# Kernel tuning notes

Measured on AMD Instinct MI355X. Metric: run time of the kernel, lower is better.

Reference implementation:

```python
import jax, jax.numpy as jnp
import numpy as np

DA, DZ, HID, IM = 5, 10, 128, 64


def _encode(x, w1, b1, w2, b2, w3, b3, wd, bd):
    # Conv2D k=4 s=2 'same' (pad 1,1) + ReLU, x3, then flatten + Dense(20)
    dn = ('NHWC', 'HWIO', 'NHWC')
    for w, b in ((w1, b1), (w2, b2), (w3, b3)):
        x = jax.lax.conv_general_dilated(x, w, (2, 2), [(1, 1), (1, 1)], dimension_numbers=dn)
        x = jax.nn.relu(x + b)
    x = x.reshape(x.shape[0], -1)
    return x @ wd + bd


def _lstm(a_in, k, rk, b):
    # keras LSTM, gate order i,f,c,o; stateful step-by-step == scan over shifted seq
    B = a_in.shape[0]
    def step(carry, x):
        h, c = carry
        g = x @ k + h @ rk + b
        gi, gf, gg, go = jnp.split(g, 4, axis=-1)
        c = jax.nn.sigmoid(gf) * c + jax.nn.sigmoid(gi) * jnp.tanh(gg)
        h = jax.nn.sigmoid(go) * jnp.tanh(c)
        return (h, c), h
    z = jnp.zeros((B, HID), a_in.dtype)
    _, hs = jax.lax.scan(step, (z, z), jnp.swapaxes(a_in, 0, 1))
    return hs  # [T, B, HID]


def _forward(images, w1, b1, w2, b2, w3, b3, wd, bd, lk, lrk, lb, wabc, babc):
    B, T = images.shape[0], images.shape[1]
    # encode all frames in one batched pass (per-frame encode is recursion-independent)
    lat = _encode(images.reshape(B * T, IM, IM, 1), w1, b1, w2, b2, w3, b3, wd, bd)
    a_all = lat[:, :DA].reshape(B, T, DA)  # encode() mean split
    # LSTM consumes a_prev: a0=zeros at t=0, then a_{t-1}
    a_in = jnp.concatenate([jnp.zeros((B, 1, DA), a_all.dtype), a_all[:, :-1]], axis=1)
    hs = _lstm(a_in, lk, lrk, lb)  # [T,B,HID]
    abc = hs @ wabc + babc  # [T,B,DZ*DZ+DA*DZ]
    A = abc[..., :DZ * DZ].reshape(T, B, DZ, DZ)
    C = abc[..., DZ * DZ:].reshape(T, B, DA, DZ)

    Q = 0.08 * jnp.eye(DZ, dtype=a_all.dtype)
    R = 0.03 * jnp.eye(DA, dtype=a_all.dtype)
    I = jnp.eye(DZ, dtype=a_all.dtype)
    std_min = 1e-4 * I

    def kf(carry, inp):
        z, P = carry
        At, Ct, at = inp
        z_hat = jnp.einsum('bij,bj->bi', At, z)
        P_hat = At @ P @ jnp.swapaxes(At, -1, -2) + Q
        resid = at - jnp.einsum('bij,bj->bi', Ct, z_hat)
        S = Ct @ P_hat @ jnp.swapaxes(Ct, -1, -2) + R
        K = P_hat @ jnp.swapaxes(Ct, -1, -2) @ jnp.linalg.inv(S)
        pz = z_hat + jnp.einsum('bij,bj->bi', K, resid)
        pP = (I - K @ Ct) @ P_hat
        # note: clamped P_hat is stored, but update() above used the unclamped one
        return (pz, pP), (z_hat, jnp.maximum(P_hat, std_min), pz, pP)

    z0 = jnp.zeros((B, DZ), a_all.dtype)
    P0 = jnp.broadcast_to(I, (B, DZ, DZ))
    _, (z_hat_s, P_hat_s, pz_s, pP_s) = jax.lax.scan(kf, (z0, P0), (A, C, jnp.swapaxes(a_all, 0, 1)))
    last_z, last_P = pz_s[-1], pP_s[-1]

    def rts(carry, inp):
        zs, Ps = carry
        pz_prev, pP_prev, Aj, zhj, Phj = inp
        D = pP_prev @ jnp.swapaxes(Aj, -1, -2) @ jnp.linalg.inv(Phj)
        zn = pz_prev + jnp.einsum('bij,bj->bi', D, zs - zhj)
        Pn = pP_prev + D @ (Ps - Phj) @ jnp.swapaxes(D, -1, -2)
        return (zn, Pn), (zn, Pn)

    # j = T-1 .. 1, reading post[j-1], A[j], z_hat[j], P_hat_clamped[j]
    rev = (pz_s[:-1][::-1], pP_s[:-1][::-1], A[1:][::-1], z_hat_s[1:][::-1], P_hat_s[1:][::-1])
    _, (zsm_r, Psm_r) = jax.lax.scan(rts, (last_z, last_P), rev)
    z_smooth = jnp.swapaxes(zsm_r[::-1], 0, 1)  # [B, T-1, DZ]
    P_smooth = jnp.swapaxes(Psm_r[::-1], 0, 1)  # [B, T-1, DZ, DZ]
    return z_smooth, P_smooth, a_all, A, C, last_z, last_P


def setup_inputs() -> dict:
    key = jax.random.key(0)
    ks = jax.random.split(key, 9)
    B, T = 3, 128
    f = lambda k, shape, s: jax.random.normal(k, shape, jnp.float32) * s
    return {
        'images': jax.random.uniform(ks[0], (B, T, IM, IM, 1), jnp.float32),
        'w1': f(ks[1], (4, 4, 1, 64), 0.25), 'b1': jnp.zeros((64,), jnp.float32),
        'w2': f(ks[2], (4, 4, 64, 128), 0.03), 'b2': jnp.zeros((128,), jnp.float32),
        'w3': f(ks[3], (4, 4, 128, 512), 0.022), 'b3': jnp.zeros((512,), jnp.float32),
        'wd': f(ks[4], (8 * 8 * 512, 20), 0.006), 'bd': jnp.zeros((20,), jnp.float32),
        'lk': f(ks[5], (DA, 4 * HID), 0.3), 'lrk': f(ks[6], (HID, 4 * HID), 0.08),
        'lb': jnp.zeros((4 * HID,), jnp.float32),
        'wabc': f(ks[7], (HID, DZ * DZ + DA * DZ), 0.02),
        'babc': jnp.zeros((DZ * DZ + DA * DZ,), jnp.float32),
    }


def reference(images, w1, b1, w2, b2, w3, b3, wd, bd, lk, lrk, lb, wabc, babc):
    return _forward(images, w1, b1, w2, b2, w3, b3, wd, bd, lk, lrk, lb, wabc, babc)
```

## Files before the change

### kernel.cpp

```cpp
#include <hip/hip_runtime.h>
#include <math.h>

typedef unsigned int   u32;
typedef unsigned short u16;
typedef short bf16x8 __attribute__((ext_vector_type(8)));
typedef float f32x4  __attribute__((ext_vector_type(4)));

#define OUT_ZS    0
#define OUT_PS    3810
#define OUT_AALL  41910
#define OUT_A     43830
#define OUT_C     82230
#define OUT_LASTZ 101430
#define OUT_LASTP 101460

__device__ __forceinline__ float sigm(float x){ return 1.f/(1.f+expf(-x)); }
__device__ __forceinline__ float safed(float d){
    return (fabsf(d) < 1e-30f) ? ((d < 0.f) ? -1e-30f : 1e-30f) : d;
}
__device__ __forceinline__ u16 f2b(float f) {
    union { float f; u32 u; } v; v.f = f;
    u32 r = v.u + 0x7fffu + ((v.u >> 16) & 1u);
    return (u16)(r >> 16);
}
__device__ __forceinline__ float b2f(u16 u) {
    union { u32 x; float f; } v; v.x = ((u32)u) << 16; return v.f;
}
__device__ __forceinline__ u32 packb(float a, float b){ return (u32)f2b(a) | ((u32)f2b(b) << 16); }

__device__ u16   r14_c1[25165824];
__device__ u16   r14_c2[12582912];
__device__ u16   r14_w2h[131072];
__device__ u16   r14_w2l[131072];
__device__ u16   r14_w3h[1048576];
__device__ u16   r14_w3l[1048576];
__device__ float r14_wdT[163840];
__device__ float r20_dpart[7680];
__device__ float r14_hs[49152];
__device__ float r14_zhat[3840];
__device__ float r14_phat[38400];
__device__ float r14_pz[3840];
__device__ float r14_pp[38400];
__device__ float r14_aall[1920];
__device__ float r14_A[38400];
__device__ float r14_C[19200];
__device__ float r14_G[38400];

__global__ __launch_bounds__(256) void conv1_r14(const float* __restrict__ img,
        const float* __restrict__ w1, const float* __restrict__ b1, u16* __restrict__ out)
{
    __shared__ float in_lds[66*66];
    const int f = blockIdx.x, tid = threadIdx.x;
    const int og = tid >> 5, sg = tid & 31;

    for (int i = tid; i < 66*66; i += 256) in_lds[i] = 0.f;
    __syncthreads();
    const float4* src = (const float4*)(img + f*4096);
    for (int i = tid; i < 1024; i += 256) {
        int r = i >> 4, c0 = (i & 15) * 4;
        float4 v = src[i];
        float* dst = &in_lds[(r+1)*66 + c0 + 1];
        dst[0]=v.x; dst[1]=v.y; dst[2]=v.z; dst[3]=v.w;
    }
    float wr[16][8];
    #pragma unroll
    for (int k = 0; k < 16; k++) {
        float4 a = *(const float4*)&w1[k*64 + og*8];
        float4 b = *(const float4*)&w1[k*64 + og*8 + 4];
        wr[k][0]=a.x; wr[k][1]=a.y; wr[k][2]=a.z; wr[k][3]=a.w;
        wr[k][4]=b.x; wr[k][5]=b.y; wr[k][6]=b.z; wr[k][7]=b.w;
    }
    float bias[8];
    #pragma unroll
    for (int j = 0; j < 8; j++) bias[j] = b1[og*8+j];
    __syncthreads();

    for (int yy = 0; yy < 32; yy++) {
        float inv[16];
        #pragma unroll
        for (int ky = 0; ky < 4; ky++)
            #pragma unroll
            for (int kx = 0; kx < 4; kx++)
                inv[ky*4+kx] = in_lds[(2*yy+ky)*66 + 2*sg+kx];
        float acc[8];
        #pragma unroll
        for (int j = 0; j < 8; j++) acc[j] = bias[j];
        #pragma unroll
        for (int k = 0; k < 16; k++)
            #pragma unroll
            for (int j = 0; j < 8; j++) acc[j] += inv[k]*wr[k][j];
        #pragma unroll
        for (int j = 0; j < 8; j++) acc[j] = fmaxf(acc[j], 0.f);
        uint4 pk = make_uint4(packb(acc[0],acc[1]), packb(acc[2],acc[3]),
                              packb(acc[4],acc[5]), packb(acc[6],acc[7]));
        *(uint4*)(out + (f*1024 + yy*32 + sg)*64 + og*8) = pk;
    }
}

__global__ __launch_bounds__(256) void w2t_r14(const float* __restrict__ w2,
        u16* __restrict__ hi, u16* __restrict__ lo)
{
    int idx = blockIdx.x*256 + threadIdx.x;
    if (idx < 131072) {
        int k = idx >> 7, oc = idx & 127;
        float v = w2[idx];
        u16 h = f2b(v);
        hi[oc*1024 + k] = h;
        lo[oc*1024 + k] = f2b(v - b2f(h));
    }
}
__global__ __launch_bounds__(256) void w3t_r14(const float* __restrict__ w3,
        u16* __restrict__ hi, u16* __restrict__ lo)
{
    int idx = blockIdx.x*256 + threadIdx.x;
    if (idx < 1048576) {
        int k = idx >> 9, oc = idx & 511;
        float v = w3[idx];
        u16 h = f2b(v);
        hi[oc*2048 + k] = h;
        lo[oc*2048 + k] = f2b(v - b2f(h));
    }
}
__global__ __launch_bounds__(256) void wdt_r14(const float* __restrict__ wd, float* __restrict__ wdT)
{
    int idx = blockIdx.x*256 + threadIdx.x;
    if (idx < 163840) {
        int j = idx & 32767, d = idx >> 15;
        wdT[d*32768 + j] = wd[j*20 + d];
    }
}

__global__ __launch_bounds__(256) void conv2_r14(const u16* __restrict__ c1b,
        const u16* __restrict__ w2h, const u16* __restrict__ w2l,
        const float* __restrict__ b2, u16* __restrict__ c2b)
{
    __shared__ __align__(16) u16 slab[128*72];
    const int f = blockIdx.x, mc = blockIdx.y, tid = threadIdx.x;
    const int wave = tid >> 6, lane = tid & 63, quad = lane >> 4, ln = lane & 15;

    f32x4 acc[8][2];
    const f32x4 zz = {0.f, 0.f, 0.f, 0.f};
    #pragma unroll
    for (int mt = 0; mt < 8; mt++) { acc[mt][0] = zz; acc[mt][1] = zz; }

    const int sp = tid >> 1;
    const int sy = mc*8 + (sp >> 4), sx = sp & 15;
    const int sic = (tid & 1) * 32;

    for (int kk = 0; kk < 16; kk++) {
        const int ky = kk >> 2, kx = kk & 3;
        __syncthreads();
        {
            int iy = 2*sy - 1 + ky, ix = 2*sx - 1 + kx;
            uint4* d4 = (uint4*)&slab[sp*72 + sic];
            if (iy >= 0 && iy < 32 && ix >= 0 && ix < 32) {
                const uint4* s4 = (const uint4*)&c1b[((f*32 + iy)*32 + ix)*64 + sic];
                d4[0]=s4[0]; d4[1]=s4[1]; d4[2]=s4[2]; d4[3]=s4[3];
            } else {
                uint4 z = make_uint4(0,0,0,0);
                d4[0]=z; d4[1]=z; d4[2]=z; d4[3]=z;
            }
        }
        __syncthreads();
        #pragma unroll
        for (int ks = 0; ks < 2; ks++) {
            bf16x8 af[8];
            #pragma unroll
            for (int mt = 0; mt < 8; mt++)
                af[mt] = *(const bf16x8*)&slab[(mt*16 + ln)*72 + ks*32 + quad*8];
            #pragma unroll
            for (int nt = 0; nt < 2; nt++) {
                const int oc = wave*32 + nt*16 + ln;
                const int kb = kk*64 + ks*32 + quad*8;
                bf16x8 bh = *(const bf16x8*)&w2h[oc*1024 + kb];
                bf16x8 bl = *(const bf16x8*)&w2l[oc*1024 + kb];
                #pragma unroll
                for (int mt = 0; mt < 8; mt++) {
                    acc[mt][nt] = __builtin_amdgcn_mfma_f32_16x16x32_bf16(af[mt], bh, acc[mt][nt], 0,0,0);
                    acc[mt][nt] = __builtin_amdgcn_mfma_f32_16x16x32_bf16(af[mt], bl, acc[mt][nt], 0,0,0);
                }
            }
        }
    }
    #pragma unroll
    for (int nt = 0; nt < 2; nt++) {
        const int oc = wave*32 + nt*16 + ln;
        const float bias = b2[oc];
        #pragma unroll
        for (int mt = 0; mt < 8; mt++)
            #pragma unroll
            for (int r = 0; r < 4; r++) {
                int pix = mc*128 + mt*16 + quad*4 + r;
                c2b[(f*256 + pix)*128 + oc] = f2b(fmaxf(acc[mt][nt][r] + bias, 0.f));
            }
    }
}

__global__ __launch_bounds__(256, 3) void conv3_r21(const u16* __restrict__ c2b,
        const u16* __restrict__ w3h, const u16* __restrict__ w3l,
        const float* __restrict__ b3)
{
    __shared__ __align__(16) u16 slab[2][64*136];
    const int fp = blockIdx.x, ocg = blockIdx.y, tid = threadIdx.x;
    const int wave = tid >> 6, lane = tid & 63, quad = lane >> 4, ln = lane & 15;
    const int wn = ocg*128 + wave*32;

    f32x4 acc[2][4][2];
    const f32x4 zz = {0.f, 0.f, 0.f, 0.f};
    #pragma unroll
    for (int f2 = 0; f2 < 2; f2++)
        #pragma unroll
        for (int mt = 0; mt < 4; mt++) { acc[f2][mt][0] = zz; acc[f2][mt][1] = zz; }

    const int sp = tid >> 2;
    const int sy = sp >> 3, sx = sp & 7;
    const int sic = (tid & 3) * 32;

    for (int kk = 0; kk < 16; kk++) {
        const int ky = kk >> 2, kx = kk & 3;
        const int iy = 2*sy - 1 + ky, ix = 2*sx - 1 + kx;
        const bool vin = (iy >= 0 && iy < 16 && ix >= 0 && ix < 16);
        __syncthreads();
        #pragma unroll
        for (int f2 = 0; f2 < 2; f2++) {
            const int f = fp*2 + f2;
            uint4* d4 = (uint4*)&slab[f2][sp*136 + sic];
            if (vin) {
                const uint4* s4 = (const uint4*)&c2b[((f*16 + iy)*16 + ix)*128 + sic];
                d4[0]=s4[0]; d4[1]=s4[1]; d4[2]=s4[2]; d4[3]=s4[3];
            } else {
                uint4 z = make_uint4(0,0,0,0);
                d4[0]=z; d4[1]=z; d4[2]=z; d4[3]=z;
            }
        }
        __syncthreads();
        #pragma unroll
        for (int ks = 0; ks < 4; ks++) {
            bf16x8 af[2][4];
            #pragma unroll
            for (int f2 = 0; f2 < 2; f2++)
                #pragma unroll
                for (int mt = 0; mt < 4; mt++)
                    af[f2][mt] = *(const bf16x8*)&slab[f2][(mt*16 + ln)*136 + ks*32 + quad*8];
            const int kb = kk*128 + ks*32 + quad*8;
            #pragma unroll
            for (int nt = 0; nt < 2; nt++) {
                const int oc = wn + nt*16 + ln;
                bf16x8 bh = *(const bf16x8*)&w3h[oc*2048 + kb];
                bf16x8 bl = *(const bf16x8*)&w3l[oc*2048 + kb];
                #pragma unroll
                for (int f2 = 0; f2 < 2; f2++)
                    #pragma unroll
                    for (int mt = 0; mt < 4; mt++) {
                        acc[f2][mt][nt] = __builtin_amdgcn_mfma_f32_16x16x32_bf16(af[f2][mt], bh, acc[f2][mt][nt], 0,0,0);
                        acc[f2][mt][nt] = __builtin_amdgcn_mfma_f32_16x16x32_bf16(af[f2][mt], bl, acc[f2][mt][nt], 0,0,0);
                    }
            }
        }
    }

    float pd[2][5];
    #pragma unroll
    for (int f2 = 0; f2 < 2; f2++)
        #pragma unroll
        for (int d = 0; d < 5; d++) pd[f2][d] = 0.f;
    #pragma unroll
    for (int nt = 0; nt < 2; nt++) {
        const int oc = wn + nt*16 + ln;
        const float bias = b3[oc];
        #pragma unroll
        for (int mt = 0; mt < 4; mt++)
            #pragma unroll
            for (int r = 0; r < 4; r++) {
                const int pix = mt*16 + quad*4 + r;
                const float* wp = &r14_wdT[pix*512 + oc];
                const float w0 = wp[0], w1 = wp[32768], w2 = wp[65536],
                            w3v = wp[98304], w4 = wp[131072];
                #pragma unroll
                for (int f2 = 0; f2 < 2; f2++) {
                    const float v = fmaxf(acc[f2][mt][nt][r] + bias, 0.f);
                    pd[f2][0] += v*w0; pd[f2][1] += v*w1; pd[f2][2] += v*w2;
                    pd[f2][3] += v*w3v; pd[f2][4] += v*w4;
                }
            }
    }
    __syncthreads();
    float* red = (float*)slab;
    #pragma unroll
    for (int f2 = 0; f2 < 2; f2++)
        #pragma unroll
        for (int d = 0; d < 5; d++) red[(f2*5+d)*256 + tid] = pd[f2][d];
    __syncthreads();
    for (int st = 128; st > 0; st >>= 1) {
        if (tid < st) {
            #pragma unroll
            for (int q = 0; q < 10; q++) red[q*256+tid] += red[q*256+tid+st];
        }
        __syncthreads();
    }
    if (tid < 10) {
        const int f2 = tid/5, d = tid%5;
        r20_dpart[((fp*2+f2)*4 + ocg)*5 + d] = red[tid*256];
    }
}

__global__ __launch_bounds__(512) void lstm_r21(const float* __restrict__ lk,
        const float* __restrict__ lrk, const float* __restrict__ lb,
        const float* __restrict__ bd, float* __restrict__ dout)
{
    const int b = blockIdx.x, c = threadIdx.x;
    __shared__ float a_lds[640];
    __shared__ float h_lds[128];
    __shared__ float g_lds[512];
    for (int i = c; i < 640; i += 512) {
        const int f = b*128 + i/5, d = i % 5;
        float v = bd[d];
        #pragma unroll
        for (int g = 0; g < 4; g++) v += r20_dpart[f*20 + g*5 + d];
        a_lds[i] = v;
        r14_aall[f*5 + d] = v;
        dout[OUT_AALL + f*5 + d] = v;
    }
    if (c < 128) h_lds[c] = 0.f;
    float wreg[128];
    #pragma unroll
    for (int j = 0; j < 128; j++) wreg[j] = lrk[j*512 + c];
    float lkr[5];
    #pragma unroll
    for (int d = 0; d < 5; d++) lkr[d] = lk[d*512 + c];
    const float gb = lb[c];
    float cs = 0.f;
    __syncthreads();
    for (int t = 0; t < 128; t++) {
        float g = gb;
        if (t > 0) {
            #pragma unroll
            for (int d = 0; d < 5; d++) g += a_lds[(t-1)*5 + d] * lkr[d];
        }
        float s0=0.f, s1=0.f, s2=0.f, s3=0.f;
        #pragma unroll
        for (int j = 0; j < 128; j += 4) {
            float4 h4 = *(const float4*)&h_lds[j];
            s0 += h4.x*wreg[j];   s1 += h4.y*wreg[j+1];
            s2 += h4.z*wreg[j+2]; s3 += h4.w*wreg[j+3];
        }
        g += (s0 + s1) + (s2 + s3);
        g_lds[c] = g;
        __syncthreads();
        if (c < 128) {
            float gi = g_lds[c], gf = g_lds[c+128], gg = g_lds[c+256], go = g_lds[c+384];
            cs = sigm(gf)*cs + sigm(gi)*tanhf(gg);
            float hn = sigm(go)*tanhf(cs);
            h_lds[c] = hn;
            r14_hs[(t*3 + b)*128 + c] = hn;
        }
        __syncthreads();
    }
}

__global__ __launch_bounds__(192) void abc_r14(const float* __restrict__ wabc,
        const float* __restrict__ babc, float* __restrict__ dout)
{
    const int tb = blockIdx.x, c = threadIdx.x;
    __shared__ float h_lds[128];
    if (c < 128) h_lds[c] = r14_hs[tb*128 + c];
    __syncthreads();
    if (c < 150) {
        float s = babc[c];
        for (int j = 0; j < 128; j++) s += h_lds[j]*wabc[j*150 + c];
        if (c < 100) { r14_A[tb*100 + c] = s; dout[OUT_A + tb*100 + c] = s; }
        else         { r14_C[tb*50 + (c-100)] = s; dout[OUT_C + tb*50 + (c-100)] = s; }
    }
}

__global__ __launch_bounds__(128) void kf_r15(float* __restrict__ dout)
{
    const int b = blockIdx.x, tid = threadIdx.x;
    const int i10 = tid/10, j10 = tid%10;
    __shared__ float Ab[2][100], Cb[2][56], avb[2][8];
    __shared__ float z[12], P[100], zh[12], AP[100], Ph[100], resid[8],
                     CPm[52], PCt[52], Ssh[28], Kg[52];

    float rA = 0.f, rC = 0.f, rav = 0.f;
    if (tid < 100) rA  = r14_A[(0*3+b)*100 + tid];
    if (tid < 50)  rC  = r14_C[(0*3+b)*50 + tid];
    if (tid < 5)   rav = r14_aall[(b*128+0)*5 + tid];
    if (tid < 100) P[tid] = (i10==j10) ? 1.f : 0.f;
    if (tid < 10)  z[tid] = 0.f;
    if (tid < 100) Ab[0][tid] = rA;
    if (tid < 50)  Cb[0][tid] = rC;
    if (tid < 5)   avb[0][tid] = rav;
    if (tid < 100) rA  = r14_A[(1*3+b)*100 + tid];
    if (tid < 50)  rC  = r14_C[(1*3+b)*50 + tid];
    if (tid < 5)   rav = r14_aall[(b*128+1)*5 + tid];
    __syncthreads();

    for (int t = 0; t < 128; t++) {
        const int cb = t & 1, nb = cb ^ 1;
        const float* Ax = Ab[cb];
        const float* Cx = Cb[cb];

        if (tid < 100) {
            float s = 0.f;
            #pragma unroll
            for (int k = 0; k < 10; k++) s += Ax[i10*10+k]*P[k*10+j10];
            AP[tid] = s;
        } else if (tid < 110) {
            const int i = tid - 100;
            float s = 0.f;
            #pragma unroll
            for (int k = 0; k < 10; k++) s += Ax[i*10+k]*z[k];
            zh[i] = s;
        }
        __syncthreads();

        if (tid < 100) {
            float s = (i10==j10) ? 0.08f : 0.f;
            #pragma unroll
            for (int k = 0; k < 10; k++) s += AP[i10*10+k]*Ax[j10*10+k];
            Ph[tid] = s;
        } else if (tid < 105) {
            const int c = tid - 100;
            float s = avb[cb][c];
            #pragma unroll
            for (int k = 0; k < 10; k++) s -= Cx[c*10+k]*zh[k];
            resid[c] = s;
        }
        __syncthreads();

        if (tid < 50) {
            const int i = tid/10, j = tid%10;
            float s = 0.f;
            #pragma unroll
            for (int k = 0; k < 10; k++) s += Cx[i*10+k]*Ph[k*10+j];
            CPm[tid] = s;
        } else if (tid >= 64 && tid < 114) {
            const int q = tid-64, i = q/5, j = q%5;
            float s = 0.f;
            #pragma unroll
            for (int k = 0; k < 10; k++) s += Ph[i*10+k]*Cx[j*10+k];
            PCt[q] = s;
        }
        __syncthreads();

        if (tid < 25) {
            const int i = tid/5, j = tid%5;
            float s = (i==j) ? 0.03f : 0.f;
            #pragma unroll
            for (int k = 0; k < 10; k++) s += CPm[i*10+k]*Cx[j*10+k];
            Ssh[tid] = s;
        }
        __syncthreads();

        if (tid < 10) {
            float M[5][5], bb[5], pv[5], x[5];
            #pragma unroll
            for (int r = 0; r < 5; r++)
                #pragma unroll
                for (int c = 0; c < 5; c++) M[r][c] = Ssh[c*5+r];
            #pragma unroll
            for (int k = 0; k < 5; k++) bb[k] = PCt[tid*5+k];
            #pragma unroll
            for (int k = 0; k < 5; k++) {
                const float p = 1.f/safed(M[k][k]);
                pv[k] = p;
                #pragma unroll
                for (int r = k+1; r < 5; r++) {
                    const float f = M[r][k]*p;
                    #pragma unroll
                    for (int c = k+1; c < 5; c++) M[r][c] -= f*M[k][c];
                    bb[r] -= f*bb[k];
                }
            }
            #pragma unroll
            for (int k = 4; k >= 0; k--) {
                float s = bb[k];
                #pragma unroll
                for (int c = k+1; c < 5; c++) s -= M[k][c]*x[c];
                x[k] = s*pv[k];
            }
            #pragma unroll
            for (int k = 0; k < 5; k++) Kg[tid*5+k] = x[k];
        }
        __syncthreads();

        if (tid < 100) {
            float s = Ph[tid];
            #pragma unroll
            for (int k = 0; k < 5; k++) s -= Kg[i10*5+k]*CPm[k*10+j10];
            r14_pp[(t*3+b)*100 + tid] = s;
            P[tid] = s;
            r14_phat[(t*3+b)*100 + tid] = fmaxf(Ph[tid], (i10==j10)?1e-4f:0.f);
            if (tid < 10) r14_zhat[(t*3+b)*10 + tid] = zh[tid];
        } else if (tid < 110) {
            const int i = tid - 100;
            float s = zh[i];
            #pragma unroll
            for (int k = 0; k < 5; k++) s += Kg[i*5+k]*resid[k];
            r14_pz[(t*3+b)*10 + i] = s;
            z[i] = s;
        }
        if (t < 127) {
            if (tid < 100) Ab[nb][tid] = rA;
            if (tid < 50)  Cb[nb][tid] = rC;
            if (tid < 5)   avb[nb][tid] = rav;
            if (t < 126) {
                if (tid < 100) rA  = r14_A[((t+2)*3+b)*100 + tid];
                if (tid < 50)  rC  = r14_C[((t+2)*3+b)*50 + tid];
                if (tid < 5)   rav = r14_aall[(b*128+(t+2))*5 + tid];
            }
        }
        __syncthreads();
    }
    if (tid < 10)  dout[OUT_LASTZ + b*10 + tid]  = z[tid];
    if (tid < 100) dout[OUT_LASTP + b*100 + tid] = P[tid];
}

__global__ __launch_bounds__(256) void ginv_r14()
{
    const int idx = blockIdx.x;
    const int tt = idx/3 + 1, b = idx%3;
    const int tid = threadIdx.x;
    __shared__ float M[10][21];
    __shared__ float A[100];
    __shared__ int piv;
    if (tid < 100) {
        int i = tid/10, j = tid%10;
        M[i][j] = r14_phat[(tt*3+b)*100 + tid];
        M[i][10+j] = (i==j) ? 1.f : 0.f;
        A[tid] = r14_A[(tt*3+b)*100 + tid];
    }
    __syncthreads();
    const int r = tid/20, cc = tid%20;
    for (int k = 0; k < 10; k++) {
        if (tid == 0) {
            int p = k; float best = fabsf(M[k][k]);
            for (int rr = k+1; rr < 10; rr++) {
                float v = fabsf(M[rr][k]);
                if (v > best) { best = v; p = rr; }
            }
            piv = p;
        }
        __syncthreads();
        if (piv != k && tid < 20) {
            float a = M[k][tid], bb = M[piv][tid];
            M[k][tid] = bb; M[piv][tid] = a;
        }
        __syncthreads();
        float pinv = 1.f/safed(M[k][k]);
        float myf = 0.f, rowv = 0.f;
        if (tid < 200) { myf = M[r][k]; rowv = M[k][cc]; }
        __syncthreads();
        if (tid < 200) {
            if (r == k) M[k][cc] = rowv*pinv;
            else        M[r][cc] -= myf*pinv*rowv;
        }
        __syncthreads();
    }
    if (tid < 100) {
        int i = tid/10, j = tid%10;
        float s = 0.f;
        #pragma unroll
        for (int k = 0; k < 10; k++) s += A[k*10+i]*M[k][10+j];
        r14_G[(tt*3+b)*100 + tid] = s;
    }
}

__global__ __launch_bounds__(128) void rts_r14(float* __restrict__ dout)
{
    const int b = blockIdx.x, tid = threadIdx.x;
    const int i10 = tid/10, j10 = tid%10;
    __shared__ float zc[10], Pc[100], D[100], Gt[100], pPm[100], ph[100],
                     zh[10], pzv[10], dz[10], T1[100], zn[10], Pnn[100];
    if (tid < 10)  zc[tid] = r14_pz[(127*3+b)*10 + tid];
    if (tid < 100) Pc[tid] = r14_pp[(127*3+b)*100 + tid];
    for (int t = 126; t >= 0; t--) {
        __syncthreads();
        if (tid < 100) {
            Gt[tid]  = r14_G[((t+1)*3+b)*100 + tid];
            pPm[tid] = r14_pp[(t*3+b)*100 + tid];
            ph[tid]  = r14_phat[((t+1)*3+b)*100 + tid];
        }
        if (tid < 10) {
            zh[tid]  = r14_zhat[((t+1)*3+b)*10 + tid];
            pzv[tid] = r14_pz[(t*3+b)*10 + tid];
        }
        __syncthreads();
        if (tid < 100){ float s=0.f; for (int k=0;k<10;k++) s += pPm[i10*10+k]*Gt[k*10+j10]; D[tid]=s; }
        if (tid < 10) dz[tid] = zc[tid] - zh[tid];
        __syncthreads();
        if (tid < 10) { float s=pzv[tid]; for (int k=0;k<10;k++) s += D[tid*10+k]*dz[k]; zn[tid]=s; }
        if (tid < 100){ float s=0.f; for (int k=0;k<10;k++) s += D[i10*10+k]*(Pc[k*10+j10]-ph[k*10+j10]); T1[tid]=s; }
        __syncthreads();
        if (tid < 100){ float s=pPm[tid]; for (int k=0;k<10;k++) s += T1[i10*10+k]*D[j10*10+k]; Pnn[tid]=s; }
        __syncthreads();
        if (tid < 10) { dout[OUT_ZS + (b*127+t)*10 + tid] = zn[tid]; zc[tid]=zn[tid]; }
        if (tid < 100){ dout[OUT_PS + (b*127+t)*100 + tid] = Pnn[tid]; Pc[tid]=Pnn[tid]; }
    }
}

extern "C" void kernel_launch(void* const* d_in, const int* in_sizes, int n_in,
                              void* d_out, int out_size, void* d_ws, size_t ws_size,
                              hipStream_t stream)
{
    (void)in_sizes; (void)n_in; (void)out_size; (void)d_ws; (void)ws_size;
    const float* images = (const float*)d_in[0];
    const float* w1   = (const float*)d_in[1];
    const float* b1   = (const float*)d_in[2];
    const float* w2   = (const float*)d_in[3];
    const float* b2   = (const float*)d_in[4];
    const float* w3   = (const float*)d_in[5];
    const float* b3   = (const float*)d_in[6];
    const float* wd   = (const float*)d_in[7];
    const float* bd   = (const float*)d_in[8];
    const float* lk   = (const float*)d_in[9];
    const float* lrk  = (const float*)d_in[10];
    const float* lb   = (const float*)d_in[11];
    const float* wabc = (const float*)d_in[12];
    const float* babc = (const float*)d_in[13];
    float* dout = (float*)d_out;

    u16 *c1p, *c2p, *w2hp, *w2lp, *w3hp, *w3lp;
    float *wdTp;
    hipGetSymbolAddress((void**)&c1p,  HIP_SYMBOL(r14_c1));
    hipGetSymbolAddress((void**)&c2p,  HIP_SYMBOL(r14_c2));
    hipGetSymbolAddress((void**)&w2hp, HIP_SYMBOL(r14_w2h));
    hipGetSymbolAddress((void**)&w2lp, HIP_SYMBOL(r14_w2l));
    hipGetSymbolAddress((void**)&w3hp, HIP_SYMBOL(r14_w3h));
    hipGetSymbolAddress((void**)&w3lp, HIP_SYMBOL(r14_w3l));
    hipGetSymbolAddress((void**)&wdTp, HIP_SYMBOL(r14_wdT));

    conv1_r14<<<dim3(384), dim3(256), 0, stream>>>(images, w1, b1, c1p);
    w2t_r14<<<dim3(512), dim3(256), 0, stream>>>(w2, w2hp, w2lp);
    w3t_r14<<<dim3(4096), dim3(256), 0, stream>>>(w3, w3hp, w3lp);
    wdt_r14<<<dim3(640), dim3(256), 0, stream>>>(wd, wdTp);
    conv2_r14<<<dim3(384, 2), dim3(256), 0, stream>>>(c1p, w2hp, w2lp, b2, c2p);
    conv3_r21<<<dim3(192, 4), dim3(256), 0, stream>>>(c2p, w3hp, w3lp, b3);
    lstm_r21<<<dim3(3), dim3(512), 0, stream>>>(lk, lrk, lb, bd, dout);
    abc_r14<<<dim3(384), dim3(192), 0, stream>>>(wabc, babc, dout);
    kf_r15<<<dim3(3), dim3(128), 0, stream>>>(dout);
    ginv_r14<<<dim3(381), dim3(256), 0, stream>>>();
    rts_r14<<<dim3(3), dim3(128), 0, stream>>>(dout);
}
```

Measured before the change: 912.3 us.

## Parallelize LSTM gate activations, overlap KF prefetch, and pipeline RTS smoother loads

The LSTM now applies each gate's sigmoid or tanh in all 512 threads before the barrier, so the 128 cell-update threads no longer evaluate four transcendentals serially. In the Kalman filter, the double-buffer stores and the next-step global prefetch move earlier, so they overlap the single-thread-group 5x5 solve. The RTS smoother is rebuilt with double-buffered LDS, register prefetch two steps ahead, fewer barriers per step, and the z update handled by otherwise idle threads. Together these target the latency of the serial recurrent kernels, at the cost of more shared memory and registers.

```diff
diff --git a/kernel.cpp b/kernel.cpp
--- a/kernel.cpp
+++ b/kernel.cpp
@@ -304,7 +304,7 @@
     }
 }
 
-__global__ __launch_bounds__(512) void lstm_r21(const float* __restrict__ lk,
+__global__ __launch_bounds__(512) void lstm_r22(const float* __restrict__ lk,
         const float* __restrict__ lrk, const float* __restrict__ lb,
         const float* __restrict__ bd, float* __restrict__ dout)
 {
@@ -329,6 +329,7 @@
     #pragma unroll
     for (int d = 0; d < 5; d++) lkr[d] = lk[d*512 + c];
     const float gb = lb[c];
+    const bool is_gg = (c >= 256 && c < 384);
     float cs = 0.f;
     __syncthreads();
     for (int t = 0; t < 128; t++) {
@@ -345,12 +346,12 @@
             s2 += h4.z*wreg[j+2]; s3 += h4.w*wreg[j+3];
         }
         g += (s0 + s1) + (s2 + s3);
-        g_lds[c] = g;
+        g_lds[c] = is_gg ? tanhf(g) : sigm(g);
         __syncthreads();
         if (c < 128) {
-            float gi = g_lds[c], gf = g_lds[c+128], gg = g_lds[c+256], go = g_lds[c+384];
-            cs = sigm(gf)*cs + sigm(gi)*tanhf(gg);
-            float hn = sigm(go)*tanhf(cs);
+            float ai = g_lds[c], af_ = g_lds[c+128], ag = g_lds[c+256], ao = g_lds[c+384];
+            cs = af_*cs + ai*ag;
+            float hn = ao*tanhf(cs);
             h_lds[c] = hn;
             r14_hs[(t*3 + b)*128 + c] = hn;
         }
@@ -373,7 +374,7 @@
     }
 }
 
-__global__ __launch_bounds__(128) void kf_r15(float* __restrict__ dout)
+__global__ __launch_bounds__(128) void kf_r22(float* __restrict__ dout)
 {
     const int b = blockIdx.x, tid = threadIdx.x;
     const int i10 = tid/10, j10 = tid%10;
@@ -452,6 +453,16 @@
         }
         __syncthreads();
 
+        if (t < 127) {
+            if (tid < 100) Ab[nb][tid] = rA;
+            if (tid < 50)  Cb[nb][tid] = rC;
+            if (tid < 5)   avb[nb][tid] = rav;
+            if (t < 126) {
+                if (tid < 100) rA  = r14_A[((t+2)*3+b)*100 + tid];
+                if (tid < 50)  rC  = r14_C[((t+2)*3+b)*50 + tid];
+                if (tid < 5)   rav = r14_aall[(b*128+(t+2))*5 + tid];
+            }
+        }
         if (tid < 10) {
             float M[5][5], bb[5], pv[5], x[5];
             #pragma unroll
@@ -499,16 +510,6 @@
             for (int k = 0; k < 5; k++) s += Kg[i*5+k]*resid[k];
             r14_pz[(t*3+b)*10 + i] = s;
             z[i] = s;
-        }
-        if (t < 127) {
-            if (tid < 100) Ab[nb][tid] = rA;
-            if (tid < 50)  Cb[nb][tid] = rC;
-            if (tid < 5)   avb[nb][tid] = rav;
-            if (t < 126) {
-                if (tid < 100) rA  = r14_A[((t+2)*3+b)*100 + tid];
-                if (tid < 50)  rC  = r14_C[((t+2)*3+b)*50 + tid];
-                if (tid < 5)   rav = r14_aall[(b*128+(t+2))*5 + tid];
-            }
         }
         __syncthreads();
     }
@@ -566,36 +567,90 @@
     }
 }
 
-__global__ __launch_bounds__(128) void rts_r14(float* __restrict__ dout)
+__global__ __launch_bounds__(128) void rts_r22(float* __restrict__ dout)
 {
     const int b = blockIdx.x, tid = threadIdx.x;
     const int i10 = tid/10, j10 = tid%10;
-    __shared__ float zc[10], Pc[100], D[100], Gt[100], pPm[100], ph[100],
-                     zh[10], pzv[10], dz[10], T1[100], zn[10], Pnn[100];
-    if (tid < 10)  zc[tid] = r14_pz[(127*3+b)*10 + tid];
+    const bool hz = (tid >= 100 && tid < 110);
+    const int zi = tid - 100;
+    __shared__ float zc[12], Pc[100], D[100], dz[12], T1[100];
+    __shared__ float Gtb[2][100], pPb[2][100], phb[2][100], zhb[2][12], pzb[2][12];
+
+    if (tid < 10) zc[tid] = r14_pz[(127*3+b)*10 + tid];
     if (tid < 100) Pc[tid] = r14_pp[(127*3+b)*100 + tid];
+
+    float g0=0.f, p0=0.f, f0=0.f, zr=0.f, pr=0.f;
+    if (tid < 100) {
+        Gtb[0][tid] = r14_G[(127*3+b)*100 + tid];
+        pPb[0][tid] = r14_pp[(126*3+b)*100 + tid];
+        phb[0][tid] = r14_phat[(127*3+b)*100 + tid];
+    }
+    if (hz) {
+        zhb[0][zi] = r14_zhat[(127*3+b)*10 + zi];
+        pzb[0][zi] = r14_pz[(126*3+b)*10 + zi];
+    }
+    if (tid < 100) {
+        g0 = r14_G[(126*3+b)*100 + tid];
+        p0 = r14_pp[(125*3+b)*100 + tid];
+        f0 = r14_phat[(126*3+b)*100 + tid];
+    }
+    if (hz) {
+        zr = r14_zhat[(126*3+b)*10 + zi];
+        pr = r14_pz[(125*3+b)*10 + zi];
+    }
+    __syncthreads();
+
     for (int t = 126; t >= 0; t--) {
-        __syncthreads();
+        const int cb = (126 - t) & 1, nb = cb ^ 1;
+
         if (tid < 100) {
-            Gt[tid]  = r14_G[((t+1)*3+b)*100 + tid];
-            pPm[tid] = r14_pp[(t*3+b)*100 + tid];
-            ph[tid]  = r14_phat[((t+1)*3+b)*100 + tid];
-        }
-        if (tid < 10) {
-            zh[tid]  = r14_zhat[((t+1)*3+b)*10 + tid];
-            pzv[tid] = r14_pz[(t*3+b)*10 + tid];
-        }
-        __syncthreads();
-        if (tid < 100){ float s=0.f; for (int k=0;k<10;k++) s += pPm[i10*10+k]*Gt[k*10+j10]; D[tid]=s; }
-        if (tid < 10) dz[tid] = zc[tid] - zh[tid];
-        __syncthreads();
-        if (tid < 10) { float s=pzv[tid]; for (int k=0;k<10;k++) s += D[tid*10+k]*dz[k]; zn[tid]=s; }
-        if (tid < 100){ float s=0.f; for (int k=0;k<10;k++) s += D[i10*10+k]*(Pc[k*10+j10]-ph[k*10+j10]); T1[tid]=s; }
-        __syncthreads();
-        if (tid < 100){ float s=pPm[tid]; for (int k=0;k<10;k++) s += T1[i10*10+k]*D[j10*10+k]; Pnn[tid]=s; }
-        __syncthreads();
-        if (tid < 10) { dout[OUT_ZS + (b*127+t)*10 + tid] = zn[tid]; zc[tid]=zn[tid]; }
-        if (tid < 100){ dout[OUT_PS + (b*127+t)*100 + tid] = Pnn[tid]; Pc[tid]=Pnn[tid]; }
+            float s = 0.f;
+            #pragma unroll
+            for (int k = 0; k < 10; k++) s += pPb[cb][i10*10+k]*Gtb[cb][k*10+j10];
+            D[tid] = s;
+        } else if (tid < 110) {
+            dz[zi] = zc[zi] - zhb[cb][zi];
+        }
+        __syncthreads();
+
+        if (tid < 100) {
+            float s = 0.f;
+            #pragma unroll
+            for (int k = 0; k < 10; k++) s += D[i10*10+k]*(Pc[k*10+j10] - phb[cb][k*10+j10]);
+            T1[tid] = s;
+        } else if (tid < 110) {
+            float s2 = pzb[cb][zi];
+            #pragma unroll
+            for (int k = 0; k < 10; k++) s2 += D[zi*10+k]*dz[k];
+            zc[zi] = s2;
+            dout[OUT_ZS + (b*127+t)*10 + zi] = s2;
+        }
+        if (t > 0) {
+            if (tid < 100) { Gtb[nb][tid] = g0; pPb[nb][tid] = p0; phb[nb][tid] = f0; }
+            if (hz)        { zhb[nb][zi] = zr; pzb[nb][zi] = pr; }
+            if (t > 1) {
+                const int s2 = t - 2;
+                if (tid < 100) {
+                    g0 = r14_G[((s2+1)*3+b)*100 + tid];
+                    p0 = r14_pp[(s2*3+b)*100 + tid];
+                    f0 = r14_phat[((s2+1)*3+b)*100 + tid];
+                }
+                if (hz) {
+                    zr = r14_zhat[((s2+1)*3+b)*10 + zi];
+                    pr = r14_pz[(s2*3+b)*10 + zi];
+                }
+            }
+        }
+        __syncthreads();
+
+        if (tid < 100) {
+            float s = pPb[cb][tid];
+            #pragma unroll
+            for (int k = 0; k < 10; k++) s += T1[i10*10+k]*D[j10*10+k];
+            dout[OUT_PS + (b*127+t)*100 + tid] = s;
+            Pc[tid] = s;
+        }
+        __syncthreads();
     }
 }
 
@@ -636,9 +691,9 @@
     wdt_r14<<<dim3(640), dim3(256), 0, stream>>>(wd, wdTp);
     conv2_r14<<<dim3(384, 2), dim3(256), 0, stream>>>(c1p, w2hp, w2lp, b2, c2p);
     conv3_r21<<<dim3(192, 4), dim3(256), 0, stream>>>(c2p, w3hp, w3lp, b3);
-    lstm_r21<<<dim3(3), dim3(512), 0, stream>>>(lk, lrk, lb, bd, dout);
+    lstm_r22<<<dim3(3), dim3(512), 0, stream>>>(lk, lrk, lb, bd, dout);
     abc_r14<<<dim3(384), dim3(192), 0, stream>>>(wabc, babc, dout);
-    kf_r15<<<dim3(3), dim3(128), 0, stream>>>(dout);
+    kf_r22<<<dim3(3), dim3(128), 0, stream>>>(dout);
     ginv_r14<<<dim3(381), dim3(256), 0, stream>>>();
-    rts_r14<<<dim3(3), dim3(128), 0, stream>>>(dout);
-}
+    rts_r22<<<dim3(3), dim3(128), 0, stream>>>(dout);
+}
```

Measured after the change: 823.3 us (median of 2 runs). 9.8% less time.
